# Optimization experiments

Measured on AMD Instinct MI355X. Metric: run time of the kernel, lower is better.

Reference implementation:

```python
import jax, jax.numpy as jnp
import numpy as np

S, T, SP = 4096, 64, 48          # spatial, temporal, seqPredict
P = T - SP                        # predictLength = 16
INP, EMB_H, EMB = 3, 64, 128      # input size, embedding hidden, embedding size
HID, OUT = 256, 128               # LSTM hidden, outputLayer size
FC1, FC2, LG = 256, 64, 32        # output FCNet dims, laneGate hidden


def setup_inputs() -> dict:
    key = jax.random.key(0)
    ks = jax.random.split(key, 32)
    def w(k, shape, fan_in):
        return jax.random.normal(k, shape, dtype=jnp.float32) / np.sqrt(fan_in)
    inp = {}
    inp["inputData"] = jax.random.normal(ks[0], (S, T, INP), dtype=jnp.float32)
    inp["lane"] = jax.random.uniform(ks[1], (S, 1), dtype=jnp.float32)
    # laneGate FCNet: 1 -> LG -> 1
    inp["lgW1"] = w(ks[2], (LG, 1), 1); inp["lgb1"] = jnp.zeros((LG,), jnp.float32)
    inp["lgW2"] = w(ks[3], (1, LG), LG); inp["lgb2"] = jnp.zeros((1,), jnp.float32)
    # embedding FCNet: INP -> EMB_H -> EMB
    inp["eW1"] = w(ks[4], (EMB_H, INP), INP); inp["eb1"] = jnp.zeros((EMB_H,), jnp.float32)
    inp["eW2"] = w(ks[5], (EMB, EMB_H), EMB_H); inp["eb2"] = jnp.zeros((EMB,), jnp.float32)
    # LSTMCell (gate order i, f, g, o)
    inp["Wih"] = w(ks[6], (4 * HID, EMB), EMB)
    inp["Whh"] = w(ks[7], (4 * HID, HID), HID)
    inp["bih"] = jnp.zeros((4 * HID,), jnp.float32)
    inp["bhh"] = jnp.zeros((4 * HID,), jnp.float32)
    # Conv1d(1,1,3,padding=1)
    inp["convw"] = w(ks[8], (3,), 3)
    inp["convb"] = jnp.zeros((1,), jnp.float32)
    # outputLayer: HID -> OUT
    inp["oW"] = w(ks[9], (OUT, HID), HID); inp["ob"] = jnp.zeros((OUT,), jnp.float32)
    # outputs FCNet (addLayer): OUT -> FC1 -> FC2 -> 1
    inp["fW1"] = w(ks[10], (FC1, OUT), OUT); inp["fb1"] = jnp.zeros((FC1,), jnp.float32)
    inp["fW2"] = w(ks[11], (FC2, FC1), FC1); inp["fb2"] = jnp.zeros((FC2,), jnp.float32)
    inp["fW3"] = w(ks[12], (1, FC2), FC2); inp["fb3"] = jnp.zeros((1,), jnp.float32)
    return inp


def reference(inputData, lane, lgW1, lgb1, lgW2, lgb2, eW1, eb1, eW2, eb2,
              Wih, Whh, bih, bhh, convw, convb, oW, ob,
              fW1, fb1, fW2, fb2, fW3, fb3):
    # laneGate: FCNet(1->LG->1) then sigmoid
    lg = jax.nn.relu(lane @ lgW1.T + lgb1) @ lgW2.T + lgb2
    laneC = jax.nn.sigmoid(lg)                       # [S, 1]
    x = inputData * laneC[:, :, None]                # [S, T, INP]
    # embedding FCNet + outer relu
    emb = jax.nn.relu(jax.nn.relu(x @ eW1.T + eb1) @ eW2.T + eb2)  # [S, T, EMB]
    xs = jnp.transpose(emb, (1, 0, 2))               # [T, S, EMB]

    def convpool(h):
        hp = jnp.pad(h, ((0, 0), (1, 1)))
        return convw[0] * hp[:, :-2] + convw[1] * hp[:, 1:-1] + convw[2] * hp[:, 2:] + convb[0]

    def step(carry, x_t):
        h, c = carry
        g = x_t @ Wih.T + bih + h @ Whh.T + bhh      # [S, 4*HID]
        i, f, gg, o = jnp.split(g, 4, axis=-1)
        c = jax.nn.sigmoid(f) * c + jax.nn.sigmoid(i) * jnp.tanh(gg)
        h = jax.nn.sigmoid(o) * jnp.tanh(c)
        h = convpool(h)
        return (h, c), (h, c)

    h0 = jnp.zeros((S, HID), jnp.float32)
    c0 = jnp.zeros((S, HID), jnp.float32)
    # loop 1: time 0 .. SP inclusive (SP+1 steps)
    (h1, c1), (Hs1, Cs1) = jax.lax.scan(step, (h0, c0), xs[:SP + 1])
    # loop 2: time SP .. T-1 (re-processes step SP, overwriting H[:,:,SP])
    (_, _), (Hs2, Cs2) = jax.lax.scan(step, (h1, c1), xs[SP:])

    H = jnp.transpose(jnp.concatenate([Hs1[:SP], Hs2], axis=0), (1, 2, 0))  # [S, HID, T]
    C = jnp.transpose(jnp.concatenate([Cs1[:SP], Cs2], axis=0), (1, 2, 0))

    predict_h = jnp.transpose(Hs2, (1, 0, 2)).reshape(S * P, HID)
    out = predict_h @ oW.T + ob                      # [S*P, OUT]
    out = jax.nn.relu(out @ fW1.T + fb1)
    out = jax.nn.relu(out @ fW2.T + fb2)
    out = out @ fW3.T + fb3                          # [S*P, 1]
    output = out.reshape(S, P) / laneC               # [S, P]
    return (output, H, C)
```

## Files before the change

kernel.cpp:

```cpp
#include <hip/hip_runtime.h>
#include <hip/hip_bf16.h>
#include <stdint.h>

using f32x4  = __attribute__((ext_vector_type(4))) float;
using bf16x8 = __attribute__((ext_vector_type(8))) __bf16;
using short8 = __attribute__((ext_vector_type(8))) short;

__device__ __forceinline__ short f2b(float f) {
    unsigned u = __builtin_bit_cast(unsigned, f);
    unsigned r = (u + 0x7fff + ((u >> 16) & 1)) >> 16;
    return (short)r;
}
__device__ __forceinline__ float b2f(short s) {
    unsigned u = ((unsigned)(unsigned short)s) << 16;
    return __builtin_bit_cast(float, u);
}
__device__ __forceinline__ float sigf(float x) {
    return __builtin_amdgcn_rcpf(1.f + __expf(-x));
}
__device__ __forceinline__ float tanhf_fast(float x) {
    x = fminf(fmaxf(x, -15.f), 15.f);
    return 2.f * __builtin_amdgcn_rcpf(1.f + __expf(-2.f * x)) - 1.f;
}

__global__ __launch_bounds__(256) void lanec_k(const float* lane, const float* W1, const float* b1,
                                               const float* W2, const float* b2, float* laneC) {
    int s = blockIdx.x * 256 + threadIdx.x;
    float v = lane[s];
    float acc = b2[0];
    #pragma unroll
    for (int k = 0; k < 32; ++k) {
        float t = fmaxf(v * W1[k] + b1[k], 0.f);
        acc += t * W2[k];
    }
    laneC[s] = 1.f / (1.f + __expf(-acc));
}

__global__ __launch_bounds__(256) void pack_k(const float* Wih, const float* Whh, const float* bih,
                                              const float* bhh, const float* oW, const float* fW1,
                                              const float* fW2, const float* eW2,
                                              short* pW, float* biasP,
                                              short* oWp, short* fW1p, short* fW2p, short* eW2p) {
    int i = blockIdx.x * 256 + threadIdx.x;
    if (i < 393216) {
        int p = i / 384, k = i % 384;
        int g = (p >> 4) & 3;
        int j = ((p >> 6) << 4) | (p & 15);
        int n = g * 256 + j;
        pW[i] = f2b(k < 128 ? Wih[n * 128 + k] : Whh[n * 256 + (k - 128)]);
        return;
    }
    i -= 393216;
    if (i < 1024) {
        int p = i;
        int g = (p >> 4) & 3;
        int j = ((p >> 6) << 4) | (p & 15);
        int n = g * 256 + j;
        biasP[p] = bih[n] + bhh[n];
        return;
    }
    i -= 1024;
    if (i < 32768) { oWp[i] = f2b(oW[i]); return; }
    i -= 32768;
    if (i < 32768) { fW1p[i] = f2b(fW1[i]); return; }
    i -= 32768;
    if (i < 32768) {
        int n = i / 256;
        fW2p[i] = (n < 64) ? f2b(fW2[i]) : (short)0;
        return;
    }
    i -= 32768;
    if (i < 8192) { eW2p[i] = f2b(eW2[i]); return; }
}

__global__ __launch_bounds__(256) void embed1_k(const float* inp, const float* laneC,
                                                const float* eW1, const float* eb1, short* h1) {
    int g = threadIdx.x >> 6, j = threadIdx.x & 63;
    int t = blockIdx.x >> 10;
    int s = ((blockIdx.x & 1023) << 2) + g;
    float lc = laneC[s];
    size_t rin = ((size_t)s * 64 + t) * 3;
    float x0 = inp[rin] * lc, x1 = inp[rin + 1] * lc, x2 = inp[rin + 2] * lc;
    float h = fmaxf(eW1[j * 3] * x0 + eW1[j * 3 + 1] * x1 + eW1[j * 3 + 2] * x2 + eb1[j], 0.f);
    h1[((size_t)t * 4096 + s) * 64 + j] = f2b(h);
}

__global__ __launch_bounds__(256) void gemm_k(const short* A1, int K1, const short* A2, int K2,
                                              const short* B, int Kt, const float* bias,
                                              float* outF, short* outB, int Nstore, int Nreal,
                                              int relu) {
    __shared__ alignas(16) short As[128 * 32];
    __shared__ alignas(16) short Bs[128 * 32];
    int tid = threadIdx.x;
    int wave = tid >> 6, lane = tid & 63;
    int m0 = blockIdx.x * 128, n0 = blockIdx.y * 128;

    f32x4 acc[4][4];
    #pragma unroll
    for (int i = 0; i < 4; ++i)
        #pragma unroll
        for (int j = 0; j < 4; ++j) acc[i][j] = (f32x4){0.f, 0.f, 0.f, 0.f};

    const int lr = lane & 15, lk8 = (lane >> 4) * 8;
    const int am = (wave & 1) * 64, bn = (wave >> 1) * 64;
    const int row = tid >> 2, c8 = (tid & 3) * 8;
    int nK = Kt / 32;

    for (int kt = 0; kt < nK; ++kt) {
        int kk = kt * 32;
        const short* Asrc; int astr, acol;
        if (kk < K1) { Asrc = A1; astr = K1; acol = kk; }
        else         { Asrc = A2; astr = K2; acol = kk - K1; }
        short8 a0 = *(const short8*)(Asrc + (size_t)(m0 + row) * astr + acol + c8);
        short8 a1 = *(const short8*)(Asrc + (size_t)(m0 + 64 + row) * astr + acol + c8);
        short8 b0 = *(const short8*)(B + (size_t)(n0 + row) * Kt + kk + c8);
        short8 b1 = *(const short8*)(B + (size_t)(n0 + 64 + row) * Kt + kk + c8);
        __syncthreads();
        *(short8*)&As[tid * 8] = a0;
        *(short8*)&As[(tid + 256) * 8] = a1;
        *(short8*)&Bs[tid * 8] = b0;
        *(short8*)&Bs[(tid + 256) * 8] = b1;
        __syncthreads();
        bf16x8 af[4], bfr[4];
        #pragma unroll
        for (int i = 0; i < 4; ++i) af[i]  = *(const bf16x8*)&As[(am + i * 16 + lr) * 32 + lk8];
        #pragma unroll
        for (int j = 0; j < 4; ++j) bfr[j] = *(const bf16x8*)&Bs[(bn + j * 16 + lr) * 32 + lk8];
        #pragma unroll
        for (int i = 0; i < 4; ++i)
            #pragma unroll
            for (int j = 0; j < 4; ++j)
                acc[i][j] = __builtin_amdgcn_mfma_f32_16x16x32_bf16(af[i], bfr[j], acc[i][j], 0, 0, 0);
    }

    int r0 = m0 + am + (lane >> 4) * 4;
    int c0 = n0 + bn + (lane & 15);
    #pragma unroll
    for (int j = 0; j < 4; ++j) {
        int col = c0 + j * 16;
        if (col >= Nreal) continue;
        float bs = bias[col];
        #pragma unroll
        for (int i = 0; i < 4; ++i) {
            #pragma unroll
            for (int r = 0; r < 4; ++r) {
                int rw = r0 + i * 16 + r;
                float v = acc[i][j][r] + bs;
                if (relu) v = fmaxf(v, 0.f);
                size_t o = (size_t)rw * Nstore + col;
                if (outF) outF[o] = v;
                if (outB) outB[o] = f2b(v);
            }
        }
    }
}

__global__ __launch_bounds__(1024) void lstm_k(const short* xs, const short* pW, const float* biasP,
                                               const float* convw, const float* convb,
                                               float* Hd, float* Cd, short* predictb, int staged) {
    __shared__ alignas(16) short A[16][392];
    __shared__ float hraw[16][258];

    const int tid = threadIdx.x;
    const int w = tid >> 6, l = tid & 63;
    const int lj = l & 15, lk = l >> 4;
    const int j = (w << 4) | lj;
    const int s4 = lk * 4;
    const int s0 = blockIdx.x * 16;

    bf16x8 wreg[4][12];
    #pragma unroll
    for (int g = 0; g < 4; ++g)
        #pragma unroll
        for (int kk = 0; kk < 12; ++kk)
            wreg[g][kk] = *(const bf16x8*)(pW + ((size_t)(64 * w + 16 * g + lj)) * 384 + kk * 32 + lk * 8);
    float bias_g[4];
    #pragma unroll
    for (int g = 0; g < 4; ++g) bias_g[g] = biasP[64 * w + 16 * g + lj];
    float creg[4] = {0.f, 0.f, 0.f, 0.f};
    const float cw0 = convw[0], cw1 = convw[1], cw2 = convw[2], cb = convb[0];

    for (int i = tid; i < 16 * 256; i += 1024) A[i >> 8][128 + (i & 255)] = 0;
    if (tid < 16) { hraw[tid][0] = 0.f; hraw[tid][257] = 0.f; }

    for (int k = 0; k < 65; ++k) {
        int it = (k <= 48) ? k : k - 1;
        {
            int r = tid >> 6, c2 = (tid & 63) * 2;
            *(int*)&A[r][c2] = *(const int*)(xs + ((size_t)it * 4096 + s0 + r) * 128 + c2);
        }
        __syncthreads();

        f32x4 acc[4];
        #pragma unroll
        for (int g = 0; g < 4; ++g) acc[g] = (f32x4){bias_g[g], bias_g[g], bias_g[g], bias_g[g]};
        #pragma unroll
        for (int kk = 0; kk < 12; ++kk) {
            bf16x8 af = *(const bf16x8*)&A[lj][kk * 32 + lk * 8];
            #pragma unroll
            for (int g = 0; g < 4; ++g)
                acc[g] = __builtin_amdgcn_mfma_f32_16x16x32_bf16(af, wreg[g][kk], acc[g], 0, 0, 0);
        }

        #pragma unroll
        for (int r = 0; r < 4; ++r) {
            float gi = acc[0][r], gf = acc[1][r], gg = acc[2][r], go = acc[3][r];
            float c = sigf(gf) * creg[r] + sigf(gi) * tanhf_fast(gg);
            creg[r] = c;
            hraw[s4 + r][j + 1] = sigf(go) * tanhf_fast(c);
        }
        __syncthreads();

        int tslot = (k < 48) ? k : k - 1;
        int doW = (k != 48);
        int pslot = k - 49;
        #pragma unroll
        for (int r = 0; r < 4; ++r) {
            int s = s4 + r;
            float h = cw0 * hraw[s][j] + cw1 * hraw[s][j + 1] + cw2 * hraw[s][j + 2] + cb;
            A[s][128 + j] = f2b(h);
            if (doW) {
                size_t o = staged ? (((size_t)(s0 + s) * 64 + tslot) * 256 + j)
                                  : (((size_t)(s0 + s) * 256 + j) * 64 + tslot);
                Hd[o] = h;
                Cd[o] = creg[r];
            }
            if (pslot >= 0) predictb[((size_t)(s0 + s) * 16 + pslot) * 256 + j] = f2b(h);
        }
    }
}

__global__ __launch_bounds__(256) void transpose_k(const float* Hs, const float* Cs,
                                                   float* Ho, float* Co) {
    __shared__ float tile[64][129];
    int s = blockIdx.x, jh = blockIdx.y;
    const float* src = blockIdx.z ? Cs : Hs;
    float* dst = blockIdx.z ? Co : Ho;
    #pragma unroll 4
    for (int i = 0; i < 32; ++i) {
        int idx = i * 256 + threadIdx.x;
        int t = idx >> 7, jj = idx & 127;
        tile[t][jj] = src[((size_t)s * 64 + t) * 256 + jh * 128 + jj];
    }
    __syncthreads();
    #pragma unroll 4
    for (int i = 0; i < 32; ++i) {
        int idx = i * 256 + threadIdx.x;
        int jj = idx >> 6, t = idx & 63;
        dst[((size_t)s * 256 + jh * 128 + jj) * 64 + t] = tile[t][jj];
    }
}

__global__ __launch_bounds__(256) void final_k(const short* t2b, const float* fW3, const float* fb3,
                                               const float* laneC, float* out0) {
    int r = blockIdx.x * 256 + threadIdx.x;
    float acc = fb3[0];
    const short* rowp = t2b + (size_t)r * 64;
    #pragma unroll 8
    for (int k = 0; k < 64; ++k) acc += b2f(rowp[k]) * fW3[k];
    out0[r] = acc / laneC[r >> 4];
}

extern "C" void kernel_launch(void* const* d_in, const int* in_sizes, int n_in,
                              void* d_out, int out_size, void* d_ws, size_t ws_size,
                              hipStream_t stream) {
    (void)in_sizes; (void)n_in; (void)out_size;
    const float* inputData = (const float*)d_in[0];
    const float* lane  = (const float*)d_in[1];
    const float* lgW1  = (const float*)d_in[2];  const float* lgb1 = (const float*)d_in[3];
    const float* lgW2  = (const float*)d_in[4];  const float* lgb2 = (const float*)d_in[5];
    const float* eW1   = (const float*)d_in[6];  const float* eb1  = (const float*)d_in[7];
    const float* eW2   = (const float*)d_in[8];  const float* eb2  = (const float*)d_in[9];
    const float* Wih   = (const float*)d_in[10]; const float* Whh  = (const float*)d_in[11];
    const float* bih   = (const float*)d_in[12]; const float* bhh  = (const float*)d_in[13];
    const float* convw = (const float*)d_in[14]; const float* convb= (const float*)d_in[15];
    const float* oW    = (const float*)d_in[16]; const float* ob   = (const float*)d_in[17];
    const float* fW1   = (const float*)d_in[18]; const float* fb1  = (const float*)d_in[19];
    const float* fW2   = (const float*)d_in[20]; const float* fb2  = (const float*)d_in[21];
    const float* fW3   = (const float*)d_in[22]; const float* fb3  = (const float*)d_in[23];

    float* out0 = (float*)d_out;
    float* Hout = out0 + 65536;
    float* Cout = Hout + (size_t)67108864;

    char* w = (char*)d_ws;
    size_t off = 0;
    auto alloc = [&](size_t bytes) -> void* {
        void* p = w + off;
        off += (bytes + 255) & ~(size_t)255;
        return p;
    };
    float* laneC    = (float*)alloc(4096 * 4);
    float* biasP    = (float*)alloc(1024 * 4);
    short* pW       = (short*)alloc((size_t)1024 * 384 * 2);
    short* oWp      = (short*)alloc((size_t)128 * 256 * 2);
    short* fW1p     = (short*)alloc((size_t)256 * 128 * 2);
    short* fW2p     = (short*)alloc((size_t)128 * 256 * 2);
    short* eW2p     = (short*)alloc((size_t)128 * 64 * 2);
    short* h1       = (short*)alloc((size_t)64 * 4096 * 64 * 2);
    short* xs       = (short*)alloc((size_t)64 * 4096 * 128 * 2);
    short* predictb = (short*)alloc((size_t)65536 * 256 * 2);
    short* t0b      = (short*)alloc((size_t)65536 * 128 * 2);
    short* t1b      = (short*)alloc((size_t)65536 * 256 * 2);
    short* t2b      = (short*)alloc((size_t)65536 * 64 * 2);
    float* Hstage   = (float*)alloc((size_t)4096 * 64 * 256 * 4);
    float* Cstage   = (float*)alloc((size_t)4096 * 64 * 256 * 4);
    bool staged = ws_size >= off;

    lanec_k<<<16, 256, 0, stream>>>(lane, lgW1, lgb1, lgW2, lgb2, laneC);
    {
        int total = 393216 + 1024 + 32768 + 32768 + 32768 + 8192;
        pack_k<<<(total + 255) / 256, 256, 0, stream>>>(Wih, Whh, bih, bhh, oW, fW1, fW2, eW2,
                                                        pW, biasP, oWp, fW1p, fW2p, eW2p);
    }
    embed1_k<<<65536, 256, 0, stream>>>(inputData, laneC, eW1, eb1, h1);
    gemm_k<<<dim3(2048, 1), 256, 0, stream>>>(h1, 64, (const short*)nullptr, 0, eW2p, 64,
                                              eb2, (float*)nullptr, xs, 128, 128, 1);

    float* Hd = staged ? Hstage : Hout;
    float* Cd = staged ? Cstage : Cout;
    lstm_k<<<256, 1024, 0, stream>>>(xs, pW, biasP, convw, convb, Hd, Cd, predictb,
                                     staged ? 1 : 0);
    if (staged)
        transpose_k<<<dim3(4096, 2, 2), 256, 0, stream>>>(Hstage, Cstage, Hout, Cout);

    gemm_k<<<dim3(512, 1), 256, 0, stream>>>(predictb, 256, (const short*)nullptr, 0, oWp, 256,
                                             ob, (float*)nullptr, t0b, 128, 128, 0);
    gemm_k<<<dim3(512, 2), 256, 0, stream>>>(t0b, 128, (const short*)nullptr, 0, fW1p, 128,
                                             fb1, (float*)nullptr, t1b, 256, 256, 1);
    gemm_k<<<dim3(512, 1), 256, 0, stream>>>(t1b, 256, (const short*)nullptr, 0, fW2p, 256,
                                             fb2, (float*)nullptr, t2b, 64, 64, 1);
    final_k<<<256, 256, 0, stream>>>(t2b, fW3, fb3, laneC, out0);
}
```

Baseline: 1.725 ms.

## Halve LSTM block size and stream recurrent weights through double-buffered LDS

The LSTM kernel moves from 1024 to 512 threads per block. Only the input-projection weights (K=0..127) stay in registers. The recurrent Whh weights are streamed each timestep from global memory into a double-buffered LDS region with async global_load_lds in 8 chunks. Weight packing is reorganised to match the new per-wave fragment layout, and x inputs are loaded straight into registers instead of staged through LDS. This cuts register pressure and thread count, at the cost of re-reading about 512KB of recurrent weights per step per block, with a barrier per chunk.

```diff
diff --git a/kernel.cpp b/kernel.cpp
--- a/kernel.cpp
+++ b/kernel.cpp
@@ -39,24 +39,27 @@
 __global__ __launch_bounds__(256) void pack_k(const float* Wih, const float* Whh, const float* bih,
                                               const float* bhh, const float* oW, const float* fW1,
                                               const float* fW2, const float* eW2,
-                                              short* pW, float* biasP,
+                                              short* pW2, float* biasP,
                                               short* oWp, short* fW1p, short* fW2p, short* eW2p) {
     int i = blockIdx.x * 256 + threadIdx.x;
     if (i < 393216) {
-        int p = i / 384, k = i % 384;
-        int g = (p >> 4) & 3;
-        int j = ((p >> 6) << 4) | (p & 15);
+        int e = i & 7, l = (i >> 3) & 63, fg = (i >> 9) & 63, kc = i >> 15;
+        int w = fg >> 3, f = fg & 7;
+        int lj = l & 15, lk = l >> 4;
+        int g = f >> 1, u = f & 1;
+        int j = 32 * w + 16 * u + lj;
         int n = g * 256 + j;
-        pW[i] = f2b(k < 128 ? Wih[n * 128 + k] : Whh[n * 256 + (k - 128)]);
+        int k = kc * 32 + lk * 8 + e;
+        pW2[i] = f2b(k < 128 ? Wih[n * 128 + k] : Whh[n * 256 + (k - 128)]);
         return;
     }
     i -= 393216;
     if (i < 1024) {
-        int p = i;
-        int g = (p >> 4) & 3;
-        int j = ((p >> 6) << 4) | (p & 15);
+        int lj = i & 15, f = (i >> 4) & 7, w = i >> 7;
+        int g = f >> 1, u = f & 1;
+        int j = 32 * w + 16 * u + lj;
         int n = g * 256 + j;
-        biasP[p] = bih[n] + bhh[n];
+        biasP[i] = bih[n] + bhh[n];
         return;
     }
     i -= 1024;
@@ -155,78 +158,123 @@
     }
 }
 
-__global__ __launch_bounds__(1024) void lstm_k(const short* xs, const short* pW, const float* biasP,
-                                               const float* convw, const float* convb,
-                                               float* Hd, float* Cd, short* predictb, int staged) {
-    __shared__ alignas(16) short A[16][392];
+__global__ __launch_bounds__(512) void lstm_k(const short* xs, const short* pW2, const float* biasP,
+                                              const float* convw, const float* convb,
+                                              float* Hd, float* Cd, short* predictb, int staged) {
+    __shared__ alignas(16) short Wbuf[2][32768];
+    __shared__ alignas(16) short h_lds[4096];
     __shared__ float hraw[16][258];
 
     const int tid = threadIdx.x;
     const int w = tid >> 6, l = tid & 63;
     const int lj = l & 15, lk = l >> 4;
-    const int j = (w << 4) | lj;
-    const int s4 = lk * 4;
     const int s0 = blockIdx.x * 16;
 
-    bf16x8 wreg[4][12];
-    #pragma unroll
-    for (int g = 0; g < 4; ++g)
-        #pragma unroll
-        for (int kk = 0; kk < 12; ++kk)
-            wreg[g][kk] = *(const bf16x8*)(pW + ((size_t)(64 * w + 16 * g + lj)) * 384 + kk * 32 + lk * 8);
-    float bias_g[4];
-    #pragma unroll
-    for (int g = 0; g < 4; ++g) bias_g[g] = biasP[64 * w + 16 * g + lj];
-    float creg[4] = {0.f, 0.f, 0.f, 0.f};
+    bf16x8 wreg[4][8];
+    #pragma unroll
+    for (int kc = 0; kc < 4; ++kc)
+        #pragma unroll
+        for (int f = 0; f < 8; ++f)
+            wreg[kc][f] = *(const bf16x8*)(pW2 + (size_t)((kc * 64 + w * 8 + f) * 64 + l) * 8);
+    float biasv[8];
+    #pragma unroll
+    for (int f = 0; f < 8; ++f) biasv[f] = biasP[w * 128 + f * 16 + lj];
+    float creg[2][4] = {{0.f, 0.f, 0.f, 0.f}, {0.f, 0.f, 0.f, 0.f}};
     const float cw0 = convw[0], cw1 = convw[1], cw2 = convw[2], cb = convb[0];
 
-    for (int i = tid; i < 16 * 256; i += 1024) A[i >> 8][128 + (i & 255)] = 0;
+    for (int i = tid; i < 4096; i += 512) h_lds[i] = 0;
     if (tid < 16) { hraw[tid][0] = 0.f; hraw[tid][257] = 0.f; }
+    __syncthreads();
+
+    short* WbufF = &Wbuf[0][0];
+    auto issue_chunk = [&](int c, int pp) {
+        const short* src = pW2 + (size_t)c * 32768 + tid * 8;
+        short* dst = WbufF + pp * 32768 + tid * 8;
+        #pragma unroll
+        for (int ri = 0; ri < 8; ++ri)
+            __builtin_amdgcn_global_load_lds(
+                (const __attribute__((address_space(1))) void*)(src + ri * 4096),
+                (__attribute__((address_space(3))) void*)(dst + ri * 4096), 16, 0, 0);
+    };
+
+    int p = 0;
+    issue_chunk(4, 0);
 
     for (int k = 0; k < 65; ++k) {
         int it = (k <= 48) ? k : k - 1;
-        {
-            int r = tid >> 6, c2 = (tid & 63) * 2;
-            *(int*)&A[r][c2] = *(const int*)(xs + ((size_t)it * 4096 + s0 + r) * 128 + c2);
+        const short* xrow = xs + ((size_t)it * 4096 + s0 + lj) * 128 + lk * 8;
+        bf16x8 ax0 = *(const bf16x8*)(xrow);
+        bf16x8 ax1 = *(const bf16x8*)(xrow + 32);
+        bf16x8 ax2 = *(const bf16x8*)(xrow + 64);
+        bf16x8 ax3 = *(const bf16x8*)(xrow + 96);
+
+        f32x4 acc[8];
+        #pragma unroll
+        for (int f = 0; f < 8; ++f) acc[f] = (f32x4){biasv[f], biasv[f], biasv[f], biasv[f]};
+        #pragma unroll
+        for (int f = 0; f < 8; ++f) acc[f] = __builtin_amdgcn_mfma_f32_16x16x32_bf16(ax0, wreg[0][f], acc[f], 0, 0, 0);
+        #pragma unroll
+        for (int f = 0; f < 8; ++f) acc[f] = __builtin_amdgcn_mfma_f32_16x16x32_bf16(ax1, wreg[1][f], acc[f], 0, 0, 0);
+        #pragma unroll
+        for (int f = 0; f < 8; ++f) acc[f] = __builtin_amdgcn_mfma_f32_16x16x32_bf16(ax2, wreg[2][f], acc[f], 0, 0, 0);
+        #pragma unroll
+        for (int f = 0; f < 8; ++f) acc[f] = __builtin_amdgcn_mfma_f32_16x16x32_bf16(ax3, wreg[3][f], acc[f], 0, 0, 0);
+
+        #pragma unroll
+        for (int cc = 0; cc < 8; ++cc) {
+            asm volatile("s_waitcnt vmcnt(0)" ::: "memory");
+            __syncthreads();
+            issue_chunk(cc < 7 ? cc + 5 : 4, p ^ 1);
+            bf16x8 ah = *(const bf16x8*)&h_lds[((cc * 4 + lk) * 16 + lj) * 8];
+            #pragma unroll
+            for (int f = 0; f < 8; ++f) {
+                bf16x8 wf = *(const bf16x8*)(WbufF + p * 32768 + ((w * 8 + f) * 64 + l) * 8);
+                acc[f] = __builtin_amdgcn_mfma_f32_16x16x32_bf16(ah, wf, acc[f], 0, 0, 0);
+            }
+            p ^= 1;
         }
-        __syncthreads();
-
-        f32x4 acc[4];
-        #pragma unroll
-        for (int g = 0; g < 4; ++g) acc[g] = (f32x4){bias_g[g], bias_g[g], bias_g[g], bias_g[g]};
-        #pragma unroll
-        for (int kk = 0; kk < 12; ++kk) {
-            bf16x8 af = *(const bf16x8*)&A[lj][kk * 32 + lk * 8];
-            #pragma unroll
-            for (int g = 0; g < 4; ++g)
-                acc[g] = __builtin_amdgcn_mfma_f32_16x16x32_bf16(af, wreg[g][kk], acc[g], 0, 0, 0);
-        }
-
-        #pragma unroll
-        for (int r = 0; r < 4; ++r) {
-            float gi = acc[0][r], gf = acc[1][r], gg = acc[2][r], go = acc[3][r];
-            float c = sigf(gf) * creg[r] + sigf(gi) * tanhf_fast(gg);
-            creg[r] = c;
-            hraw[s4 + r][j + 1] = sigf(go) * tanhf_fast(c);
-        }
-        __syncthreads();
 
         int tslot = (k < 48) ? k : k - 1;
         int doW = (k != 48);
         int pslot = k - 49;
         #pragma unroll
-        for (int r = 0; r < 4; ++r) {
-            int s = s4 + r;
-            float h = cw0 * hraw[s][j] + cw1 * hraw[s][j + 1] + cw2 * hraw[s][j + 2] + cb;
-            A[s][128 + j] = f2b(h);
-            if (doW) {
-                size_t o = staged ? (((size_t)(s0 + s) * 64 + tslot) * 256 + j)
-                                  : (((size_t)(s0 + s) * 256 + j) * 64 + tslot);
-                Hd[o] = h;
-                Cd[o] = creg[r];
+        for (int u = 0; u < 2; ++u) {
+            int j = 32 * w + 16 * u + lj;
+            #pragma unroll
+            for (int r = 0; r < 4; ++r) {
+                int s = 4 * lk + r;
+                float gi = acc[0 + u][r], gf = acc[2 + u][r];
+                float gg = acc[4 + u][r], go = acc[6 + u][r];
+                float c = sigf(gf) * creg[u][r] + sigf(gi) * tanhf_fast(gg);
+                creg[u][r] = c;
+                hraw[s][j + 1] = sigf(go) * tanhf_fast(c);
+                if (doW) {
+                    size_t o = staged ? ((((size_t)(s0 + s) * 64 + tslot) << 8) + j)
+                                      : ((((size_t)(s0 + s) << 8) + j) * 64 + tslot);
+                    Cd[o] = c;
+                }
             }
-            if (pslot >= 0) predictb[((size_t)(s0 + s) * 16 + pslot) * 256 + j] = f2b(h);
         }
+        __syncthreads();
+
+        #pragma unroll
+        for (int u = 0; u < 2; ++u) {
+            int j = 32 * w + 16 * u + lj;
+            int elbase = ((w * 4 + 2 * u + (lj >> 3)) * 16) * 8 + (lj & 7);
+            #pragma unroll
+            for (int r = 0; r < 4; ++r) {
+                int s = 4 * lk + r;
+                float h = cw0 * hraw[s][j] + cw1 * hraw[s][j + 1] + cw2 * hraw[s][j + 2] + cb;
+                h_lds[elbase + s * 8] = f2b(h);
+                if (doW) {
+                    size_t o = staged ? ((((size_t)(s0 + s) * 64 + tslot) << 8) + j)
+                                      : ((((size_t)(s0 + s) << 8) + j) * 64 + tslot);
+                    Hd[o] = h;
+                }
+                if (pslot >= 0) predictb[(((size_t)(s0 + s) * 16 + pslot) << 8) + j] = f2b(h);
+            }
+        }
+        __syncthreads();
     }
 }
 
@@ -292,7 +340,7 @@
     };
     float* laneC    = (float*)alloc(4096 * 4);
     float* biasP    = (float*)alloc(1024 * 4);
-    short* pW       = (short*)alloc((size_t)1024 * 384 * 2);
+    short* pW2      = (short*)alloc((size_t)1024 * 384 * 2);
     short* oWp      = (short*)alloc((size_t)128 * 256 * 2);
     short* fW1p     = (short*)alloc((size_t)256 * 128 * 2);
     short* fW2p     = (short*)alloc((size_t)128 * 256 * 2);
@@ -311,7 +359,7 @@
     {
         int total = 393216 + 1024 + 32768 + 32768 + 32768 + 8192;
         pack_k<<<(total + 255) / 256, 256, 0, stream>>>(Wih, Whh, bih, bhh, oW, fW1, fW2, eW2,
-                                                        pW, biasP, oWp, fW1p, fW2p, eW2p);
+                                                        pW2, biasP, oWp, fW1p, fW2p, eW2p);
     }
     embed1_k<<<65536, 256, 0, stream>>>(inputData, laneC, eW1, eb1, h1);
     gemm_k<<<dim3(2048, 1), 256, 0, stream>>>(h1, 64, (const short*)nullptr, 0, eW2p, 64,
@@ -319,8 +367,8 @@
 
     float* Hd = staged ? Hstage : Hout;
     float* Cd = staged ? Cstage : Cout;
-    lstm_k<<<256, 1024, 0, stream>>>(xs, pW, biasP, convw, convb, Hd, Cd, predictb,
-                                     staged ? 1 : 0);
+    lstm_k<<<256, 512, 0, stream>>>(xs, pW2, biasP, convw, convb, Hd, Cd, predictb,
+                                    staged ? 1 : 0);
     if (staged)
         transpose_k<<<dim3(4096, 2, 2), 256, 0, stream>>>(Hstage, Cstage, Hout, Cout);
 
```

Measured after the change: 1.832 ms. 6.3% more time.
